# Performance work log

Hardware: AMD Instinct MI355X
Metric: run time of the kernel (lower is better)

The kernel has to match this reference:

```python
import jax, jax.numpy as jnp
import numpy as np

B, C, H, W_SP = 16, 128, 112, 112  # C doubles as nb_steps (time axis)
KH = 3
TAU_MEM = 1e-3
TAU_SYN = 1e-3
TIME_STEP = 1e-3
ALPHA = float(np.exp(-TIME_STEP / TAU_SYN))
BETA = float(np.exp(-TIME_STEP / TAU_MEM))


def setup_inputs() -> dict:
    key = jax.random.key(0)
    k1, k2 = jax.random.split(key)
    x = jax.random.normal(k1, (B, C, H, W_SP), dtype=jnp.float32)
    # kaiming_uniform_(a=0, mode='fan_in', nonlinearity='linear'): bound = sqrt(3) * 1/sqrt(fan_in)
    fan_in = C * KH * KH
    bound = float(np.sqrt(3.0 / fan_in))
    W = jax.random.uniform(k2, (C, C, KH, KH), minval=-bound, maxval=bound, dtype=jnp.float32)
    b = jnp.zeros((C,), dtype=jnp.float32)
    return {"x": x, "W": W, "b": b}


def reference(x, W, b):
    # Conv2d(in_channel, in_channel, kernel=3, stride=1, padding=1)
    y = jax.lax.conv_general_dilated(
        x, W, window_strides=(1, 1), padding=((1, 1), (1, 1)),
        dimension_numbers=("NCHW", "OIHW", "NCHW")) + b[None, :, None, None]
    conv_shape = y.shape
    Bsz, T = y.shape[0], y.shape[1]  # T == nb_steps (channel axis reused as time)
    X = y.reshape(Bsz, T, -1)  # (B, T, H*W)
    # FFT of leakage kernels: l = alpha^t, k = beta^t * (1 - beta)
    t = jnp.arange(T, dtype=jnp.float32)
    l = jnp.power(jnp.float32(ALPHA), t)
    k = jnp.power(jnp.float32(BETA), t) * (1.0 - jnp.float32(BETA))
    fft_l_k = jnp.fft.rfft(l, n=2 * T) * jnp.fft.rfft(k, n=2 * T)  # (T+1,)
    # Parallel leaky integration via linear (causal) convolution in frequency domain
    fft_X = jnp.fft.rfft(X, n=2 * T, axis=1)  # (B, T+1, H*W) complex
    mem = jnp.fft.irfft(fft_X * fft_l_k[None, :, None], n=2 * T, axis=1)[:, :T]
    return mem.reshape(conv_shape)
```

## Files before the change

### kernel.cpp

```cpp
#include <hip/hip_runtime.h>

typedef __attribute__((ext_vector_type(8))) short s16x8;
typedef __attribute__((ext_vector_type(8))) unsigned short u16x8;
typedef __attribute__((ext_vector_type(4))) float f32x4;

#define ALPHA_F 0.36787944117144233f
#define BETA_F  0.36787944117144233f
#define OMB_F   0.63212055882855767f

#define XS_PSTR  40
#define XS_RSTR  720
#define XS_U16   7200
#define YS_STRIDE 130

#define X2_CICSTR 415872u
#define X2_BZSTR  1663488u

__device__ __forceinline__ unsigned short f2bf(float f){
  union { float f; unsigned int u; } v; v.f = f;
  unsigned int u = v.u;
  return (unsigned short)((u + 0x7FFFu + ((u >> 16) & 1u)) >> 16);
}
__device__ __forceinline__ float bf2f(unsigned short s){
  union { unsigned int u; float f; } v; v.u = ((unsigned int)s) << 16;
  return v.f;
}

__global__ __launch_bounds__(256) void reorder_w(const float* __restrict__ W,
                                                 unsigned short* __restrict__ Wr){
  int f = blockIdx.x * 256 + threadIdx.x;
  if (f >= 9*128*128) return;
  int cil = f & 31;
  int co  = (f >> 5) & 127;
  int cic = (f >> 12) & 3;
  int pos = f >> 14;
  int ci  = (cic << 5) | cil;
  Wr[f] = f2bf(W[(co*128 + ci)*9 + pos]);
}

__global__ __launch_bounds__(256) void convert_x(const float* __restrict__ x,
                                                 unsigned short* __restrict__ x2){
  __shared__ float ls[112*33 + 1];
  const int tid = threadIdx.x;
  const int h = blockIdx.x, cic = blockIdx.y, bz = blockIdx.z;
  const float* src = x + ((size_t)(bz*128 + cic*32))*12544 + (size_t)h*112;
  #pragma unroll
  for (int r = 0; r < 7; ++r){
    int u2 = r*256 + tid;
    int ci = u2 / 56, w2 = (u2 - ci*56) << 1;
    float2 v = *(const float2*)(src + (size_t)ci*12544 + w2);
    ls[w2*33 + ci] = v.x;
    ls[(w2+1)*33 + ci] = v.y;
  }
  __syncthreads();
  unsigned short* dst = x2 + (size_t)(bz*4 + cic)*X2_CICSTR + (size_t)(h+1)*(114*32);
  #pragma unroll
  for (int r = 0; r < 7; ++r){
    int u2 = r*256 + tid;
    int pw = u2 >> 4, c2 = (u2 & 15) << 1;
    ushort2 o;
    o.x = f2bf(ls[pw*33 + c2]);
    o.y = f2bf(ls[pw*33 + c2 + 1]);
    *(ushort2*)(dst + (pw+1)*32 + c2) = o;
  }
  if (tid < 64){
    int cil = tid & 31;
    dst[((tid >> 5) ? 113*32 : 0) + cil] = 0;
  }
  if (h == 0 || h == 111){
    unsigned short* brow = x2 + (size_t)(bz*4 + cic)*X2_CICSTR
                              + (size_t)(h == 0 ? 0 : 113)*(114*32);
    for (int u = tid; u < 114*32; u += 256) brow[u] = 0;
  }
}

template<int MODE>
__global__ __launch_bounds__(256, 4) void conv_lif(
    const float* __restrict__ x,
    const unsigned short* __restrict__ x2,
    const unsigned short* __restrict__ Wr,
    const float* __restrict__ bias,
    float* __restrict__ out)
{
  __shared__ unsigned short sm[128*YS_STRIDE];
  const int tid  = threadIdx.x;
  const int lane = tid & 63;
  const int wid  = tid >> 6;
  const int l15  = lane & 15;
  const int quad = lane >> 4;
  const int bz = blockIdx.z;
  const int h0 = blockIdx.y * 8, w0 = blockIdx.x * 16;

  const float* xb = x + (size_t)bz * 1605632;
  const unsigned short* x2b = x2 + (size_t)bz * X2_BZSTR;

  int  g_off[3], g_ci0[3], g_idx[3];
  bool g_val[3];
  #pragma unroll
  for (int it = 0; it < 3; ++it){
    int u = tid + it*256;
    bool act = (u < 720);
    int uu = act ? u : 0;
    int pos = uu >> 2, cq = uu & 3;
    int row = pos / 18, col = pos - row*18;
    if (MODE == 0){
      int gh = h0 - 1 + row, gw = w0 - 1 + col;
      bool val = act && (gh >= 0) && (gh < 112) && (gw >= 0) && (gw < 112);
      g_off[it] = val ? (gh*112 + gw) : 0;
      g_ci0[it] = cq << 3;
      g_val[it] = val;
      g_idx[it] = 0;
    } else {
      g_idx[it] = ((h0 + row)*114 + (w0 + col))*32 + (cq << 3);
      g_val[it] = act;
      g_off[it] = 0; g_ci0[it] = 0;
    }
  }

  u16x8 g[3];
  #define GATHER(cic_) do{ \
    if (MODE == 0){ \
      _Pragma("unroll") \
      for (int it = 0; it < 3; ++it){ \
        const float* p = xb + (size_t)(g_ci0[it] + ((cic_) << 5)) * 12544 + g_off[it]; \
        u16x8 v; \
        _Pragma("unroll") \
        for (int k = 0; k < 8; ++k){ \
          float f = p[(size_t)k * 12544]; \
          f = g_val[it] ? f : 0.0f; \
          v[k] = f2bf(f); \
        } \
        g[it] = v; \
      } \
    } else { \
      _Pragma("unroll") \
      for (int it = 0; it < 3; ++it){ \
        if (g_val[it]) \
          g[it] = *(const u16x8*)(x2b + (size_t)(cic_)*X2_CICSTR + g_idx[it]); \
      } \
    } }while(0)

  #define WBUF(buf_) do{ \
    unsigned short* xw = sm + (buf_)*XS_U16; \
    _Pragma("unroll") \
    for (int it = 0; it < 3; ++it){ \
      int u = tid + it*256; \
      if (u < 720) *(u16x8*)(xw + (u >> 2)*XS_PSTR + ((u & 3) << 3)) = g[it]; \
    } }while(0)

  f32x4 acc[2][8];
  #pragma unroll
  for (int i = 0; i < 2; ++i)
    #pragma unroll
    for (int j = 0; j < 8; ++j) acc[i][j] = (f32x4){0.f,0.f,0.f,0.f};

  GATHER(0); WBUF(0);

  for (int cic = 0; cic < 4; ++cic){
    __syncthreads();
    const unsigned short* xs = sm + (cic & 1)*XS_U16;
    #pragma unroll
    for (int dw = 0; dw < 3; ++dw){
      s16x8 af[3][2];
      #pragma unroll
      for (int dh = 0; dh < 3; ++dh){
        const unsigned short* wp = Wr + ((((dh*3 + dw) << 2) + cic) << 12)
                                      + (((wid << 5) + l15) << 5) + (quad << 3);
        af[dh][0] = *(const s16x8*)wp;
        af[dh][1] = *(const s16x8*)(wp + 512);
      }
      const unsigned short* bcol = xs + (l15 + dw)*XS_PSTR + (quad << 3);
      s16x8 R[6];
      #pragma unroll
      for (int r = 0; r < 4; ++r) R[r] = *(const s16x8*)(bcol + r*XS_RSTR);
      #pragma unroll
      for (int p = 0; p < 4; ++p){
        if (p < 3){
          R[(2*p+4) % 6] = *(const s16x8*)(bcol + (2*p+4)*XS_RSTR);
          R[(2*p+5) % 6] = *(const s16x8*)(bcol + (2*p+5)*XS_RSTR);
        }
        #pragma unroll
        for (int dh = 0; dh < 3; ++dh){
          #pragma unroll
          for (int sub = 0; sub < 2; ++sub){
            int nt = 2*p + sub;
            s16x8 b = R[(nt + dh) % 6];
            acc[0][nt] = __builtin_amdgcn_mfma_f32_16x16x32_bf16(af[dh][0], b, acc[0][nt], 0, 0, 0);
            acc[1][nt] = __builtin_amdgcn_mfma_f32_16x16x32_bf16(af[dh][1], b, acc[1][nt], 0, 0, 0);
          }
        }
      }
      if (dw == 1 && cic < 3) GATHER(cic+1);
    }
    if (cic < 3) WBUF((cic+1) & 1);
  }

  __syncthreads();
  #pragma unroll
  for (int mt = 0; mt < 2; ++mt){
    int cobase = (wid << 5) + (mt << 4) + (quad << 2);
    float4 bv = *(const float4*)(bias + cobase);
    #pragma unroll
    for (int nt = 0; nt < 8; ++nt){
      int pix = (nt << 4) + l15;
      f32x4 a = acc[mt][nt];
      ushort2 w01, w23;
      w01.x = f2bf(a.x + bv.x);
      w01.y = f2bf(a.y + bv.y);
      w23.x = f2bf(a.z + bv.z);
      w23.y = f2bf(a.w + bv.w);
      unsigned short* yp = sm + pix*YS_STRIDE + cobase;
      *(ushort2*)(yp)     = w01;
      *(ushort2*)(yp + 2) = w23;
    }
  }
  __syncthreads();

  {
    int pix  = tid & 127;
    int half = tid >> 7;
    int r = pix >> 4, c = pix & 15;
    float s = 0.f, m = 0.f;
    float* op = out + (size_t)bz*1605632 + (h0 + r)*112 + (w0 + c);
    const unsigned short* yr = sm + pix*YS_STRIDE;
    int t0     = half ? 48 : 0;
    int tstore = half ? 64 : 0;
    int tend   = half ? 128 : 64;
    for (int t = t0; t < tend; ++t){
      float y = bf2f(yr[t]);
      s = ALPHA_F * s + y;
      m = BETA_F  * m + OMB_F * s;
      if (t >= tstore) op[(size_t)t*12544] = m;
    }
  }
  #undef GATHER
  #undef WBUF
}

extern "C" void kernel_launch(void* const* d_in, const int* in_sizes, int n_in,
                              void* d_out, int out_size, void* d_ws, size_t ws_size,
                              hipStream_t stream){
  const float* x = (const float*)d_in[0];
  const float* W = (const float*)d_in[1];
  const float* b = (const float*)d_in[2];
  float* out = (float*)d_out;
  unsigned short* Wr = (unsigned short*)d_ws;
  reorder_w<<<576, 256, 0, stream>>>(W, Wr);

  const size_t x2_off  = 294912;
  const size_t x2_size = (size_t)16 * X2_BZSTR * 2;
  if (ws_size >= x2_off + x2_size){
    unsigned short* x2 = (unsigned short*)d_ws + x2_off/2;
    convert_x<<<dim3(112, 4, 16), 256, 0, stream>>>(x, x2);
    conv_lif<1><<<dim3(7, 14, 16), 256, 0, stream>>>(x, x2, Wr, b, out);
  } else {
    conv_lif<0><<<dim3(7, 14, 16), 256, 0, stream>>>(x, nullptr, Wr, b, out);
  }
}
```

Baseline: 268.0 us.

## Stream input tiles directly to LDS and shrink LDS to raise occupancy

```diff
diff --git a/kernel.cpp b/kernel.cpp
--- a/kernel.cpp
+++ b/kernel.cpp
@@ -8,13 +8,15 @@
 #define BETA_F  0.36787944117144233f
 #define OMB_F   0.63212055882855767f
 
-#define XS_PSTR  40
-#define XS_RSTR  720
-#define XS_U16   7200
-#define YS_STRIDE 130
+#define XS_U16   6144
+#define XS_RSTR  576
+#define YS_STRIDE 66
 
 #define X2_CICSTR 415872u
 #define X2_BZSTR  1663488u
+
+typedef __attribute__((address_space(1))) const unsigned int gu32;
+typedef __attribute__((address_space(3))) unsigned int lu32;
 
 __device__ __forceinline__ unsigned short f2bf(float f){
   union { float f; unsigned int u; } v; v.f = f;
@@ -75,14 +77,14 @@
 }
 
 template<int MODE>
-__global__ __launch_bounds__(256, 4) void conv_lif(
+__global__ __launch_bounds__(256, 6) void conv_lif(
     const float* __restrict__ x,
     const unsigned short* __restrict__ x2,
     const unsigned short* __restrict__ Wr,
     const float* __restrict__ bias,
     float* __restrict__ out)
 {
-  __shared__ unsigned short sm[128*YS_STRIDE];
+  __shared__ unsigned short sm[2*XS_U16];
   const int tid  = threadIdx.x;
   const int lane = tid & 63;
   const int wid  = tid >> 6;
@@ -111,33 +113,26 @@
       g_val[it] = val;
       g_idx[it] = 0;
     } else {
-      g_idx[it] = ((h0 + row)*114 + (w0 + col))*32 + (cq << 3);
+      g_idx[it] = act ? (((h0 + row)*114 + (w0 + col))*32 + (cq << 3)) : 0;
       g_val[it] = act;
       g_off[it] = 0; g_ci0[it] = 0;
     }
   }
+  const int ldsb0 = (wid << 6) << 3;
 
   u16x8 g[3];
-  #define GATHER(cic_) do{ \
-    if (MODE == 0){ \
+  #define GATHER_REG(cic_) do{ \
+    _Pragma("unroll") \
+    for (int it = 0; it < 3; ++it){ \
+      const float* p = xb + (size_t)(g_ci0[it] + ((cic_) << 5)) * 12544 + g_off[it]; \
+      u16x8 v; \
       _Pragma("unroll") \
-      for (int it = 0; it < 3; ++it){ \
-        const float* p = xb + (size_t)(g_ci0[it] + ((cic_) << 5)) * 12544 + g_off[it]; \
-        u16x8 v; \
-        _Pragma("unroll") \
-        for (int k = 0; k < 8; ++k){ \
-          float f = p[(size_t)k * 12544]; \
-          f = g_val[it] ? f : 0.0f; \
-          v[k] = f2bf(f); \
-        } \
-        g[it] = v; \
+      for (int k = 0; k < 8; ++k){ \
+        float f = p[(size_t)k * 12544]; \
+        f = g_val[it] ? f : 0.0f; \
+        v[k] = f2bf(f); \
       } \
-    } else { \
-      _Pragma("unroll") \
-      for (int it = 0; it < 3; ++it){ \
-        if (g_val[it]) \
-          g[it] = *(const u16x8*)(x2b + (size_t)(cic_)*X2_CICSTR + g_idx[it]); \
-      } \
+      g[it] = v; \
     } }while(0)
 
   #define WBUF(buf_) do{ \
@@ -145,7 +140,15 @@
     _Pragma("unroll") \
     for (int it = 0; it < 3; ++it){ \
       int u = tid + it*256; \
-      if (u < 720) *(u16x8*)(xw + (u >> 2)*XS_PSTR + ((u & 3) << 3)) = g[it]; \
+      if (u < 720) *(u16x8*)(xw + u*8) = g[it]; \
+    } }while(0)
+
+  #define GATHER_LDS(cic_, buf_) do{ \
+    _Pragma("unroll") \
+    for (int it = 0; it < 3; ++it){ \
+      const unsigned short* srcp = x2b + (size_t)(cic_)*X2_CICSTR + g_idx[it]; \
+      __builtin_amdgcn_global_load_lds((gu32*)srcp, \
+          (lu32*)(sm + (buf_)*XS_U16 + ldsb0 + it*2048), 16, 0, 0); \
     } }while(0)
 
   f32x4 acc[2][8];
@@ -154,7 +157,8 @@
     #pragma unroll
     for (int j = 0; j < 8; ++j) acc[i][j] = (f32x4){0.f,0.f,0.f,0.f};
 
-  GATHER(0); WBUF(0);
+  if (MODE == 1){ GATHER_LDS(0, 0); }
+  else          { GATHER_REG(0); WBUF(0); }
 
   for (int cic = 0; cic < 4; ++cic){
     __syncthreads();
@@ -169,7 +173,12 @@
         af[dh][0] = *(const s16x8*)wp;
         af[dh][1] = *(const s16x8*)(wp + 512);
       }
-      const unsigned short* bcol = xs + (l15 + dw)*XS_PSTR + (quad << 3);
+      if (MODE == 1 && dw == 2 && cic < 3){
+        __builtin_amdgcn_sched_barrier(0);
+        GATHER_LDS(cic+1, (cic+1) & 1);
+      }
+      if (MODE == 0 && dw == 1 && cic < 3) GATHER_REG(cic+1);
+      const unsigned short* bcol = xs + ((l15 + dw) << 5) + (quad << 3);
       s16x8 R[6];
       #pragma unroll
       for (int r = 0; r < 4; ++r) R[r] = *(const s16x8*)(bcol + r*XS_RSTR);
@@ -190,50 +199,61 @@
           }
         }
       }
-      if (dw == 1 && cic < 3) GATHER(cic+1);
     }
-    if (cic < 3) WBUF((cic+1) & 1);
+    if (MODE == 0 && cic < 3) WBUF((cic+1) & 1);
   }
 
   __syncthreads();
-  #pragma unroll
-  for (int mt = 0; mt < 2; ++mt){
-    int cobase = (wid << 5) + (mt << 4) + (quad << 2);
-    float4 bv = *(const float4*)(bias + cobase);
-    #pragma unroll
-    for (int nt = 0; nt < 8; ++nt){
-      int pix = (nt << 4) + l15;
-      f32x4 a = acc[mt][nt];
-      ushort2 w01, w23;
-      w01.x = f2bf(a.x + bv.x);
-      w01.y = f2bf(a.y + bv.y);
-      w23.x = f2bf(a.z + bv.z);
-      w23.y = f2bf(a.w + bv.w);
-      unsigned short* yp = sm + pix*YS_STRIDE + cobase;
-      *(ushort2*)(yp)     = w01;
-      *(ushort2*)(yp + 2) = w23;
-    }
-  }
-  __syncthreads();
-
   {
     int pix  = tid & 127;
     int half = tid >> 7;
     int r = pix >> 4, c = pix & 15;
     float s = 0.f, m = 0.f;
     float* op = out + (size_t)bz*1605632 + (h0 + r)*112 + (w0 + c);
-    const unsigned short* yr = sm + pix*YS_STRIDE;
     int t0     = half ? 48 : 0;
     int tstore = half ? 64 : 0;
     int tend   = half ? 128 : 64;
-    for (int t = t0; t < tend; ++t){
-      float y = bf2f(yr[t]);
-      s = ALPHA_F * s + y;
-      m = BETA_F  * m + OMB_F * s;
-      if (t >= tstore) op[(size_t)t*12544] = m;
+
+    #pragma unroll
+    for (int part = 0; part < 2; ++part){
+      if ((wid >> 1) == part){
+        #pragma unroll
+        for (int mt = 0; mt < 2; ++mt){
+          int co = (wid << 5) + (mt << 4) + (quad << 2);
+          int cl = co - (part << 6);
+          float4 bv = *(const float4*)(bias + co);
+          #pragma unroll
+          for (int nt = 0; nt < 8; ++nt){
+            int wpix = (nt << 4) + l15;
+            f32x4 a = acc[mt][nt];
+            ushort2 w01, w23;
+            w01.x = f2bf(a.x + bv.x);
+            w01.y = f2bf(a.y + bv.y);
+            w23.x = f2bf(a.z + bv.z);
+            w23.y = f2bf(a.w + bv.w);
+            unsigned short* yp = sm + wpix*YS_STRIDE + cl;
+            *(ushort2*)(yp)     = w01;
+            *(ushort2*)(yp + 2) = w23;
+          }
+        }
+      }
+      __syncthreads();
+      {
+        int lo = t0 > (part << 6) ? t0 : (part << 6);
+        int hi = tend < ((part+1) << 6) ? tend : ((part+1) << 6);
+        const unsigned short* yr = sm + pix*YS_STRIDE - (part << 6);
+        for (int t = lo; t < hi; ++t){
+          float y = bf2f(yr[t]);
+          s = ALPHA_F * s + y;
+          m = BETA_F  * m + OMB_F * s;
+          if (t >= tstore) op[(size_t)t*12544] = m;
+        }
+      }
+      if (part == 0) __syncthreads();
     }
   }
-  #undef GATHER
+  #undef GATHER_REG
+  #undef GATHER_LDS
   #undef WBUF
 }
 
```

After: 454.9 us. 69.7% more time.
